# Optimization experiments

Hardware: AMD Instinct MI355X
Metric: run time of the kernel (lower is better)

The kernel has to match this reference:

```python
import jax, jax.numpy as jnp
import numpy as np
import math

D_MODEL = 512
N_HEADS = 8
HEAD_DIM = D_MODEL // N_HEADS


def setup_inputs() -> dict:
    key = jax.random.key(0)
    k1, k2, k3 = jax.random.split(key, 3)
    B, T = 2, 4096
    x = jax.random.normal(k1, (B, T, D_MODEL), dtype=jnp.float32)
    # nn.Linear weights: stored as [out, in], applied as x @ W.T
    W_QKV = jax.random.normal(k2, (3 * D_MODEL, D_MODEL), dtype=jnp.float32) * (1.0 / math.sqrt(D_MODEL))
    W_O = jax.random.normal(k3, (D_MODEL, D_MODEL), dtype=jnp.float32) * (1.0 / math.sqrt(D_MODEL))
    return {"x": x, "W_QKV": W_QKV, "W_O": W_O}


def reference(x, W_QKV, W_O):
    B, T, C = x.shape
    qkv = (x @ W_QKV.T).reshape(B, T, 3, N_HEADS, HEAD_DIM)
    q, k, v = qkv[:, :, 0], qkv[:, :, 1], qkv[:, :, 2]  # [B,T,H,D]
    # scores: [B,H,T,T]
    scale = math.sqrt(HEAD_DIM)
    attn = jnp.einsum('bqhd,bkhd->bhqk', q, k) / scale
    causal_mask = jnp.triu(jnp.ones((T, T), dtype=bool), k=1)
    attn = jnp.where(causal_mask, -jnp.inf, attn)
    attn = jax.nn.softmax(attn, axis=-1)
    out = jnp.einsum('bhqk,bkhd->bqhd', attn, v).reshape(B, T, C)
    return out @ W_O.T
```

## Files before the change

### kernel.cpp

```cpp
#include <hip/hip_runtime.h>
#include <hip/hip_bf16.h>

typedef __bf16 bf16_t;
typedef __bf16 bf16x8 __attribute__((ext_vector_type(8)));
typedef __bf16 bf16x4 __attribute__((ext_vector_type(4)));
typedef float  floatx4 __attribute__((ext_vector_type(4)));

static __device__ __forceinline__ floatx4 mfma16(bf16x8 a, bf16x8 b, floatx4 c) {
  return __builtin_amdgcn_mfma_f32_16x16x32_bf16(a, b, c, 0, 0, 0);
}

typedef __attribute__((address_space(3))) void lds_vp;
typedef __attribute__((address_space(1))) void glb_vp;
#define GLDS16(g, l) \
  __builtin_amdgcn_global_load_lds((glb_vp*)(g), (lds_vp*)(l), 16, 0, 0)

__global__ void cvt_all_kernel(const float* __restrict__ x,
                               const float* __restrict__ wqkv,
                               const float* __restrict__ wo,
                               bf16_t* __restrict__ xb,
                               bf16_t* __restrict__ wqkvb,
                               bf16_t* __restrict__ wob) {
  int i = blockIdx.x * blockDim.x + threadIdx.x;
  const float4* src; bf16x4* dst; int off;
  if (i < 1048576)      { src = (const float4*)x;    dst = (bf16x4*)xb;    off = i; }
  else if (i < 1245184) { src = (const float4*)wqkv; dst = (bf16x4*)wqkvb; off = i - 1048576; }
  else                  { src = (const float4*)wo;   dst = (bf16x4*)wob;   off = i - 1245184; }
  float4 v = src[off];
  bf16x4 o;
  o[0] = (bf16_t)v.x; o[1] = (bf16_t)v.y; o[2] = (bf16_t)v.z; o[3] = (bf16_t)v.w;
  dst[off] = o;
}

__global__ __launch_bounds__(256) void gemm_qkv(
    const bf16_t* __restrict__ A, const bf16_t* __restrict__ B,
    bf16_t* __restrict__ Qo, bf16_t* __restrict__ Ko, bf16_t* __restrict__ Vto)
{
  __shared__ __align__(16) bf16_t As[2][128 * 64];
  __shared__ __align__(16) bf16_t Bs[2][128 * 64];
  const int tid  = threadIdx.x;
  const int lane = tid & 63;
  const int w    = tid >> 6;
  const int quad = lane >> 4;
  const int l15  = lane & 15;
  const int l7   = lane & 7;
  const int wm   = w & 1;
  const int wn   = w >> 1;
  const int K    = 512;

  floatx4 acc[4][4];
  #pragma unroll
  for (int i = 0; i < 4; ++i)
    #pragma unroll
    for (int j = 0; j < 4; ++j)
      acc[i][j] = (floatx4){0.f, 0.f, 0.f, 0.f};

  const bf16_t* Ab = A + (size_t)blockIdx.x * 128 * K;
  const bf16_t* Bb = B + (size_t)blockIdx.y * 128 * K;

  auto stage = [&](int buf, int k0) {
    #pragma unroll
    for (int i = 0; i < 4; ++i) {
      int c = tid + 256 * i;
      int row = c >> 3, colc = c & 7;
      int gofs = ((colc ^ (row & 7)) << 3);
      GLDS16(&Ab[(size_t)row * K + k0 + gofs], &As[buf][c * 8]);
      GLDS16(&Bb[(size_t)row * K + k0 + gofs], &Bs[buf][c * 8]);
    }
  };

  stage(0, 0);
  for (int it = 0; it < 8; ++it) {
    const int cur = it & 1;
    __syncthreads();
    if (it + 1 < 8) stage(cur ^ 1, (it + 1) << 6);
    #pragma unroll
    for (int ks = 0; ks < 2; ++ks) {
      bf16x8 af[4], bfr[4];
      #pragma unroll
      for (int t = 0; t < 4; ++t) {
        af[t]  = *(const bf16x8*)&As[cur][(wm * 64 + t * 16 + l15) * 64 +
                                         (((ks * 4 + quad) ^ l7) << 3)];
        bfr[t] = *(const bf16x8*)&Bs[cur][(wn * 64 + t * 16 + l15) * 64 +
                                         (((ks * 4 + quad) ^ l7) << 3)];
      }
      #pragma unroll
      for (int mt = 0; mt < 4; ++mt)
        #pragma unroll
        for (int nt = 0; nt < 4; ++nt)
          acc[mt][nt] = mfma16(af[mt], bfr[nt], acc[mt][nt]);
    }
  }

  if (blockIdx.y < 8) {
    #pragma unroll
    for (int mt = 0; mt < 4; ++mt) {
      #pragma unroll
      for (int nt = 0; nt < 4; ++nt) {
        #pragma unroll
        for (int r = 0; r < 4; ++r) {
          int m = blockIdx.x * 128 + wm * 64 + mt * 16 + quad * 4 + r;
          int n = blockIdx.y * 128 + wn * 64 + nt * 16 + l15;
          float v = acc[mt][nt][r];
          int b = m >> 12, t = m & 4095;
          int h = (n >> 6) & 7, d = n & 63;
          size_t bh = (size_t)(b * 8 + h);
          if (n < 512)
            Qo[bh * 262144 + (size_t)t * 64 + d] = (bf16_t)(v * 0.18033688f);
          else
            Ko[bh * 262144 +
               (size_t)((((t >> 4) * 2 + (d >> 5)) * 512) +
                        ((((d & 31) >> 3) * 16 + (t & 15)) * 8) + (d & 7))] =
                (bf16_t)v;
        }
      }
    }
  } else {
    __syncthreads();
    bf16_t* L = &As[0][0];
    #pragma unroll
    for (int mt = 0; mt < 4; ++mt)
      #pragma unroll
      for (int nt = 0; nt < 4; ++nt) {
        int n_l = wn * 64 + nt * 16 + l15;
        int mc  = wm * 8 + mt * 2 + (quad >> 1);
        bf16x4 v4;
        #pragma unroll
        for (int r = 0; r < 4; ++r) v4[r] = (bf16_t)acc[mt][nt][r];
        *(bf16x4*)&L[n_l * 128 + ((mc ^ (n_l & 15)) << 3) + (quad & 1) * 4] = v4;
      }
    __syncthreads();
    const int t0 = (blockIdx.x & 31) * 128;
    const int b  = blockIdx.x >> 5;
    #pragma unroll
    for (int i = 0; i < 8; ++i) {
      int c = tid + 256 * i;
      int n_l = c >> 4, tc = c & 15;
      int h = ((blockIdx.y - 8) << 1) | (n_l >> 6);
      int d = n_l & 63;
      size_t bh = (size_t)(b * 8 + h);
      int base0 = (tc >> 2) * 32 + (tc & 3) * 4;
      bf16x4 lo = *(const bf16x4*)&L[n_l * 128 +
                     (((base0 >> 3) ^ (n_l & 15)) << 3) + (base0 & 7)];
      bf16x4 hi = *(const bf16x4*)&L[n_l * 128 +
                     ((((base0 + 16) >> 3) ^ (n_l & 15)) << 3) + (base0 & 7)];
      bf16x8 o;
      #pragma unroll
      for (int e = 0; e < 4; ++e) { o[e] = lo[e]; o[e + 4] = hi[e]; }
      int T = t0 + tc * 8;
      *(bf16x8*)&Vto[bh * 262144 +
                     (size_t)((((T >> 5) * 4 + (d >> 4)) * 512) +
                              ((((T >> 3) & 3) * 16 + (d & 15)) * 8))] = o;
    }
  }
}

__global__ __launch_bounds__(256) void gemm_out(
    const bf16_t* __restrict__ A, const bf16_t* __restrict__ B,
    float* __restrict__ Cf)
{
  __shared__ __align__(16) bf16_t As[2][64 * 64];
  __shared__ __align__(16) bf16_t Bs[2][128 * 64];
  const int tid  = threadIdx.x;
  const int lane = tid & 63;
  const int w    = tid >> 6;
  const int quad = lane >> 4;
  const int l15  = lane & 15;
  const int l7   = lane & 7;

  floatx4 acc[4][2];
  #pragma unroll
  for (int i = 0; i < 4; ++i)
    #pragma unroll
    for (int j = 0; j < 2; ++j)
      acc[i][j] = (floatx4){0.f, 0.f, 0.f, 0.f};

  const bf16_t* Ab = A + (size_t)blockIdx.x * 64 * 512;
  const bf16_t* Bb = B + (size_t)blockIdx.y * 128 * 512;

  auto stage = [&](int buf, int k0) {
    #pragma unroll
    for (int i = 0; i < 2; ++i) {
      int c = tid + 256 * i;
      int row = c >> 3, colc = c & 7;
      GLDS16(&Ab[(size_t)row * 512 + k0 + ((colc ^ (row & 7)) << 3)],
             &As[buf][c * 8]);
    }
    #pragma unroll
    for (int i = 0; i < 4; ++i) {
      int c = tid + 256 * i;
      int row = c >> 3, colc = c & 7;
      GLDS16(&Bb[(size_t)row * 512 + k0 + ((colc ^ (row & 7)) << 3)],
             &Bs[buf][c * 8]);
    }
  };

  stage(0, 0);
  for (int it = 0; it < 8; ++it) {
    const int cur = it & 1;
    __syncthreads();
    if (it + 1 < 8) stage(cur ^ 1, (it + 1) << 6);
    #pragma unroll
    for (int ks = 0; ks < 2; ++ks) {
      bf16x8 af[4], bfr[2];
      #pragma unroll
      for (int t = 0; t < 4; ++t)
        af[t]  = *(const bf16x8*)&As[cur][(t * 16 + l15) * 64 +
                                         (((ks * 4 + quad) ^ l7) << 3)];
      #pragma unroll
      for (int t = 0; t < 2; ++t)
        bfr[t] = *(const bf16x8*)&Bs[cur][(w * 32 + t * 16 + l15) * 64 +
                                         (((ks * 4 + quad) ^ l7) << 3)];
      #pragma unroll
      for (int mt = 0; mt < 4; ++mt)
        #pragma unroll
        for (int nt = 0; nt < 2; ++nt)
          acc[mt][nt] = mfma16(af[mt], bfr[nt], acc[mt][nt]);
    }
  }

  #pragma unroll
  for (int mt = 0; mt < 4; ++mt)
    #pragma unroll
    for (int nt = 0; nt < 2; ++nt)
      #pragma unroll
      for (int r = 0; r < 4; ++r) {
        int m = blockIdx.x * 64 + mt * 16 + quad * 4 + r;
        int n = blockIdx.y * 128 + w * 32 + nt * 16 + l15;
        Cf[(size_t)m * 512 + n] = acc[mt][nt][r];
      }
}

__global__ __launch_bounds__(512, 1) void attn_kernel(
    const bf16_t* __restrict__ Qg, const bf16_t* __restrict__ Kf,
    const bf16_t* __restrict__ Vf, bf16_t* __restrict__ Og)
{
  __shared__ __align__(16) bf16_t smem[66560];

  const int tid  = threadIdx.x;
  const int lane = tid & 63;
  const int w    = tid >> 6;
  const int qh   = w >> 2;
  const int kq   = w & 3;
  const int quad = lane >> 4;
  const int l15  = lane & 15;

  const int id = blockIdx.x;
  const int bh = 2 * (id & 7) + ((id >> 3) & 1);
  const int x  = id >> 4;
  const int qtA = 31 - x, qtB = x;
  const size_t bh_off = (size_t)bh * 262144;
  const int b = bh >> 3, h = bh & 7;

  const bf16_t* Kb_ = Kf + bh_off;
  const bf16_t* Vb_ = Vf + bh_off;
  const floatx4 z4 = (floatx4){0.f, 0.f, 0.f, 0.f};
  bf16x8 ones;
  #pragma unroll
  for (int i = 0; i < 8; ++i) ones[i] = (bf16_t)1.0f;

  for (int ph = 0; ph < 2; ++ph) {
    const int qt   = ph ? qtB : qtA;
    const int q64  = 2 * qt + qh;
    const int qbase = qt * 128 + qh * 64;

    bf16x8 aq0[4], aq1[4];
    #pragma unroll
    for (int qb = 0; qb < 4; ++qb) {
      const bf16_t* Qp = Qg + bh_off + (size_t)(qbase + qb * 16 + l15) * 64;
      aq0[qb] = *(const bf16x8*)&Qp[quad * 8];
      aq1[qb] = *(const bf16x8*)&Qp[32 + quad * 8];
    }

    floatx4 acc_o[4][4], acc_l[4];
    #pragma unroll
    for (int qb = 0; qb < 4; ++qb) {
      #pragma unroll
      for (int dt = 0; dt < 4; ++dt) acc_o[qb][dt] = (floatx4){0.f, 0.f, 0.f, 0.f};
      acc_l[qb] = (floatx4){0.f, 0.f, 0.f, 0.f};
    }

    for (int k64 = kq; k64 <= q64; k64 += 4) {
      const bf16_t* Kp = Kb_ + (size_t)k64 * 4096;
      const bf16_t* Vp = Vb_ + (size_t)k64 * 4096;
      bf16x8 bk0[4], bk1[4];
      #pragma unroll
      for (int nt = 0; nt < 4; ++nt) {
        bk0[nt] = *(const bf16x8*)&Kp[(nt * 2 + 0) * 512 + lane * 8];
        bk1[nt] = *(const bf16x8*)&Kp[(nt * 2 + 1) * 512 + lane * 8];
      }
      floatx4 s[4][4];
      #pragma unroll
      for (int nt = 0; nt < 4; ++nt) {
        s[0][nt] = mfma16(bk0[nt], aq0[0], z4);
        s[1][nt] = mfma16(bk0[nt], aq0[1], z4);
        s[2][nt] = mfma16(bk0[nt], aq0[2], z4);
        s[3][nt] = mfma16(bk0[nt], aq0[3], z4);
      }
      #pragma unroll
      for (int nt = 0; nt < 4; ++nt)
        #pragma unroll
        for (int qb = 0; qb < 4; ++qb)
          s[qb][nt] = mfma16(bk1[nt], aq1[qb], s[qb][nt]);
      bf16x8 av[2][4];
      #pragma unroll
      for (int kc = 0; kc < 2; ++kc)
        #pragma unroll
        for (int dt = 0; dt < 4; ++dt)
          av[kc][dt] = *(const bf16x8*)&Vp[(kc * 4 + dt) * 512 + lane * 8];
      if (k64 == q64) {
        #pragma unroll
        for (int qb = 0; qb < 4; ++qb)
          #pragma unroll
          for (int nt = 0; nt < 4; ++nt)
            #pragma unroll
            for (int r = 0; r < 4; ++r)
              if (nt * 16 + quad * 4 + r > qb * 16 + l15)
                s[qb][nt][r] = -3.0e38f;
      }
      #pragma unroll
      for (int qb = 0; qb < 4; ++qb)
        #pragma unroll
        for (int nt = 0; nt < 4; ++nt)
          #pragma unroll
          for (int r = 0; r < 4; ++r)
            s[qb][nt][r] = __builtin_amdgcn_exp2f(s[qb][nt][r]);
      #pragma unroll
      for (int kc = 0; kc < 2; ++kc) {
        bf16x8 pb[4];
        #pragma unroll
        for (int qb = 0; qb < 4; ++qb)
          #pragma unroll
          for (int r = 0; r < 4; ++r) {
            pb[qb][r]     = (bf16_t)s[qb][kc * 2][r];
            pb[qb][r + 4] = (bf16_t)s[qb][kc * 2 + 1][r];
          }
        #pragma unroll
        for (int qb = 0; qb < 4; ++qb)
          acc_l[qb] = mfma16(ones, pb[qb], acc_l[qb]);
        #pragma unroll
        for (int dt = 0; dt < 4; ++dt)
          #pragma unroll
          for (int qb = 0; qb < 4; ++qb)
            acc_o[qb][dt] = mfma16(av[kc][dt], pb[qb], acc_o[qb][dt]);
      }
    }

    {
      float* Pq = (float*)&smem[0] + (qh * 4 + kq) * 4096;
      float* PL = (float*)&smem[65536];
      #pragma unroll
      for (int qb = 0; qb < 4; ++qb) {
        int q = qb * 16 + l15;
        #pragma unroll
        for (int dt = 0; dt < 4; ++dt)
          *(floatx4*)&Pq[q * 64 + (((dt * 4 + quad) ^ l15) << 2)] = acc_o[qb][dt];
        if (quad == 0) PL[(qh * 4 + kq) * 64 + q] = acc_l[qb][0];
      }
    }
    __syncthreads();
    #pragma unroll
    for (int i = 0; i < 2; ++i) {
      int a = tid + 512 * i;
      int qh_e = a >> 9, rem = a & 511;
      int q = rem >> 3, c8 = rem & 7;
      const float* Pq = (const float*)&smem[0] + qh_e * 16384;
      const float* PL = (const float*)&smem[65536] + qh_e * 256;
      float s0[8] = {0.f, 0.f, 0.f, 0.f, 0.f, 0.f, 0.f, 0.f};
      float suml = 0.f;
      #pragma unroll
      for (int k2 = 0; k2 < 4; ++k2) {
        const float* Pk = Pq + k2 * 4096 + q * 64;
        floatx4 u0 = *(const floatx4*)&Pk[((c8 * 2)     ^ (q & 15)) << 2];
        floatx4 u1 = *(const floatx4*)&Pk[((c8 * 2 + 1) ^ (q & 15)) << 2];
        #pragma unroll
        for (int r = 0; r < 4; ++r) { s0[r] += u0[r]; s0[4 + r] += u1[r]; }
        suml += PL[k2 * 64 + q];
      }
      float rl = 1.0f / suml;
      bf16x8 o;
      #pragma unroll
      for (int e = 0; e < 8; ++e) o[e] = (bf16_t)(s0[e] * rl);
      int row = qt * 128 + qh_e * 64 + q;
      *(bf16x8*)&Og[((size_t)b * 4096 + row) * 512 + h * 64 + c8 * 8] = o;
    }
    if (ph == 0) __syncthreads();
  }
}

extern "C" void kernel_launch(void* const* d_in, const int* in_sizes, int n_in,
                              void* d_out, int out_size, void* d_ws, size_t ws_size,
                              hipStream_t stream) {
  const float* x    = (const float*)d_in[0];
  const float* wqkv = (const float*)d_in[1];
  const float* wo   = (const float*)d_in[2];
  float* out = (float*)d_out;

  char* ws = (char*)d_ws;
  bf16_t* xb    = (bf16_t*)(ws);
  bf16_t* wqkvb = (bf16_t*)(ws + 8388608);
  bf16_t* wob   = (bf16_t*)(ws + 9961472);
  bf16_t* Qb    = (bf16_t*)(ws + 10485760);
  bf16_t* Kfb   = (bf16_t*)(ws + 18874368);
  bf16_t* Vfb   = (bf16_t*)(ws + 27262976);
  bf16_t* Ob    = xb;

  cvt_all_kernel<<<5120, 256, 0, stream>>>(x, wqkv, wo, xb, wqkvb, wob);

  gemm_qkv<<<dim3(64, 12), 256, 0, stream>>>(xb, wqkvb, Qb, Kfb, Vfb);
  attn_kernel<<<dim3(256), 512, 0, stream>>>(Qb, Kfb, Vfb, Ob);
  gemm_out<<<dim3(128, 4), 256, 0, stream>>>(Ob, wob, out);
}
```

Before: 144.8 us.

## Split attention work across 8 KV-slices per 64-row query tile with 512 blocks

Each attention block now owns a single 64-row query tile per phase instead of a 128-row pair, and all eight waves split the key range (stride 8) rather than two query halves with four key slices each. The grid doubles to 512 blocks, and the launch bound is raised to allow multiple blocks per CU. Shared memory is roughly halved by reducing the partial outputs in two head-dimension halves with extra barriers. The aim is better load balance and occupancy across the GPU, at the cost of more cross-wave reductions and synchronization, and Q/K reuse across waves within a block.

Result: slower. 457.2 us (+215.8%).

```diff
diff --git a/kernel.cpp b/kernel.cpp
--- a/kernel.cpp
+++ b/kernel.cpp
@@ -231,24 +231,22 @@
       }
 }
 
-__global__ __launch_bounds__(512, 1) void attn_kernel(
+__global__ __launch_bounds__(512, 4) void attn_kernel(
     const bf16_t* __restrict__ Qg, const bf16_t* __restrict__ Kf,
     const bf16_t* __restrict__ Vf, bf16_t* __restrict__ Og)
 {
-  __shared__ __align__(16) bf16_t smem[66560];
+  __shared__ __align__(16) bf16_t smem[33792];
 
   const int tid  = threadIdx.x;
   const int lane = tid & 63;
-  const int w    = tid >> 6;
-  const int qh   = w >> 2;
-  const int kq   = w & 3;
+  const int kq   = tid >> 6;
   const int quad = lane >> 4;
   const int l15  = lane & 15;
 
   const int id = blockIdx.x;
   const int bh = 2 * (id & 7) + ((id >> 3) & 1);
-  const int x  = id >> 4;
-  const int qtA = 31 - x, qtB = x;
+  const int y  = id >> 4;
+  const int q64A = 63 - y, q64B = y;
   const size_t bh_off = (size_t)bh * 262144;
   const int b = bh >> 3, h = bh & 7;
 
@@ -260,9 +258,8 @@
   for (int i = 0; i < 8; ++i) ones[i] = (bf16_t)1.0f;
 
   for (int ph = 0; ph < 2; ++ph) {
-    const int qt   = ph ? qtB : qtA;
-    const int q64  = 2 * qt + qh;
-    const int qbase = qt * 128 + qh * 64;
+    const int q64 = ph ? q64B : q64A;
+    const int qbase = q64 * 64;
 
     bf16x8 aq0[4], aq1[4];
     #pragma unroll
@@ -280,7 +277,7 @@
       acc_l[qb] = (floatx4){0.f, 0.f, 0.f, 0.f};
     }
 
-    for (int k64 = kq; k64 <= q64; k64 += 4) {
+    for (int k64 = kq; k64 <= q64; k64 += 8) {
       const bf16_t* Kp = Kb_ + (size_t)k64 * 4096;
       const bf16_t* Vp = Vb_ + (size_t)k64 * 4096;
       bf16x8 bk0[4], bk1[4];
@@ -346,45 +343,46 @@
       }
     }
 
-    {
-      float* Pq = (float*)&smem[0] + (qh * 4 + kq) * 4096;
-      float* PL = (float*)&smem[65536];
-      #pragma unroll
-      for (int qb = 0; qb < 4; ++qb) {
-        int q = qb * 16 + l15;
-        #pragma unroll
-        for (int dt = 0; dt < 4; ++dt)
-          *(floatx4*)&Pq[q * 64 + (((dt * 4 + quad) ^ l15) << 2)] = acc_o[qb][dt];
-        if (quad == 0) PL[(qh * 4 + kq) * 64 + q] = acc_l[qb][0];
-      }
-    }
-    __syncthreads();
-    #pragma unroll
-    for (int i = 0; i < 2; ++i) {
-      int a = tid + 512 * i;
-      int qh_e = a >> 9, rem = a & 511;
-      int q = rem >> 3, c8 = rem & 7;
-      const float* Pq = (const float*)&smem[0] + qh_e * 16384;
-      const float* PL = (const float*)&smem[65536] + qh_e * 256;
-      float s0[8] = {0.f, 0.f, 0.f, 0.f, 0.f, 0.f, 0.f, 0.f};
-      float suml = 0.f;
-      #pragma unroll
-      for (int k2 = 0; k2 < 4; ++k2) {
-        const float* Pk = Pq + k2 * 4096 + q * 64;
-        floatx4 u0 = *(const floatx4*)&Pk[((c8 * 2)     ^ (q & 15)) << 2];
-        floatx4 u1 = *(const floatx4*)&Pk[((c8 * 2 + 1) ^ (q & 15)) << 2];
-        #pragma unroll
-        for (int r = 0; r < 4; ++r) { s0[r] += u0[r]; s0[4 + r] += u1[r]; }
-        suml += PL[k2 * 64 + q];
-      }
-      float rl = 1.0f / suml;
-      bf16x8 o;
-      #pragma unroll
-      for (int e = 0; e < 8; ++e) o[e] = (bf16_t)(s0[e] * rl);
-      int row = qt * 128 + qh_e * 64 + q;
-      *(bf16x8*)&Og[((size_t)b * 4096 + row) * 512 + h * 64 + c8 * 8] = o;
-    }
-    if (ph == 0) __syncthreads();
+    #pragma unroll
+    for (int hd = 0; hd < 2; ++hd) {
+      if (ph | hd) __syncthreads();
+      {
+        float* Pw  = (float*)&smem[0] + kq * 2048;
+        float* PLw = (float*)&smem[32768];
+        #pragma unroll
+        for (int qb = 0; qb < 4; ++qb) {
+          int q = qb * 16 + l15;
+          #pragma unroll
+          for (int t = 0; t < 2; ++t) {
+            int cw = (t * 4 + quad) ^ (q & 7);
+            *(floatx4*)&Pw[q * 32 + cw * 4] = acc_o[qb][hd * 2 + t];
+          }
+          if (hd == 0 && quad == 0) PLw[kq * 64 + q] = acc_l[qb][0];
+        }
+      }
+      __syncthreads();
+      {
+        int q = tid >> 3, c = tid & 7;
+        const float* PB = (const float*)&smem[0];
+        const float* PL = (const float*)&smem[32768];
+        floatx4 ssum = (floatx4){0.f, 0.f, 0.f, 0.f};
+        float suml = 0.f;
+        #pragma unroll
+        for (int k = 0; k < 8; ++k) {
+          const float* Pk = PB + k * 2048 + q * 32;
+          floatx4 u = *(const floatx4*)&Pk[(c ^ (q & 7)) * 4];
+          #pragma unroll
+          for (int r = 0; r < 4; ++r) ssum[r] += u[r];
+          suml += PL[k * 64 + q];
+        }
+        float rl = 1.0f / suml;
+        bf16x4 o4;
+        #pragma unroll
+        for (int r = 0; r < 4; ++r) o4[r] = (bf16_t)(ssum[r] * rl);
+        int row = qbase + q;
+        *(bf16x4*)&Og[((size_t)b * 4096 + row) * 512 + h * 64 + hd * 32 + c * 4] = o4;
+      }
+    }
   }
 }
 
@@ -408,6 +406,6 @@
   cvt_all_kernel<<<5120, 256, 0, stream>>>(x, wqkv, wo, xb, wqkvb, wob);
 
   gemm_qkv<<<dim3(64, 12), 256, 0, stream>>>(xb, wqkvb, Qb, Kfb, Vfb);
-  attn_kernel<<<dim3(256), 512, 0, stream>>>(Qb, Kfb, Vfb, Ob);
+  attn_kernel<<<dim3(512), 512, 0, stream>>>(Qb, Kfb, Vfb, Ob);
   gemm_out<<<dim3(128, 4), 256, 0, stream>>>(Ob, wob, out);
 }
```

## Fuse fp32-to-bf16 conversion of x into the QKV GEMM A-tile load

Applied to the files above, without the earlier changes.

The x activation is no longer converted to bf16 by a separate pass. The QKV GEMM now loads fp32 x tiles into registers, converts them, and writes them into swizzled LDS after the MFMA loop, as a register-staged software pipeline. Only the weights still go through a smaller conversion kernel. This removes an 8 MB write and read of bf16 x, but each of the 12 column blocks now reads x as fp32 (twice the bytes), and the kernel uses more registers and VALU work.

Result: slower. 152.7 us (+5.5%).

```diff
diff --git a/kernel.cpp b/kernel.cpp
--- a/kernel.cpp
+++ b/kernel.cpp
@@ -15,17 +15,14 @@
 #define GLDS16(g, l) \
   __builtin_amdgcn_global_load_lds((glb_vp*)(g), (lds_vp*)(l), 16, 0, 0)
 
-__global__ void cvt_all_kernel(const float* __restrict__ x,
-                               const float* __restrict__ wqkv,
-                               const float* __restrict__ wo,
-                               bf16_t* __restrict__ xb,
-                               bf16_t* __restrict__ wqkvb,
-                               bf16_t* __restrict__ wob) {
+__global__ void cvt_w_kernel(const float* __restrict__ wqkv,
+                             const float* __restrict__ wo,
+                             bf16_t* __restrict__ wqkvb,
+                             bf16_t* __restrict__ wob) {
   int i = blockIdx.x * blockDim.x + threadIdx.x;
   const float4* src; bf16x4* dst; int off;
-  if (i < 1048576)      { src = (const float4*)x;    dst = (bf16x4*)xb;    off = i; }
-  else if (i < 1245184) { src = (const float4*)wqkv; dst = (bf16x4*)wqkvb; off = i - 1048576; }
-  else                  { src = (const float4*)wo;   dst = (bf16x4*)wob;   off = i - 1245184; }
+  if (i < 196608) { src = (const float4*)wqkv; dst = (bf16x4*)wqkvb; off = i; }
+  else            { src = (const float4*)wo;   dst = (bf16x4*)wob;   off = i - 196608; }
   float4 v = src[off];
   bf16x4 o;
   o[0] = (bf16_t)v.x; o[1] = (bf16_t)v.y; o[2] = (bf16_t)v.z; o[3] = (bf16_t)v.w;
@@ -33,7 +30,7 @@
 }
 
 __global__ __launch_bounds__(256) void gemm_qkv(
-    const bf16_t* __restrict__ A, const bf16_t* __restrict__ B,
+    const float* __restrict__ A, const bf16_t* __restrict__ B,
     bf16_t* __restrict__ Qo, bf16_t* __restrict__ Ko, bf16_t* __restrict__ Vto)
 {
   __shared__ __align__(16) bf16_t As[2][128 * 64];
@@ -55,25 +52,51 @@
     for (int j = 0; j < 4; ++j)
       acc[i][j] = (floatx4){0.f, 0.f, 0.f, 0.f};
 
-  const bf16_t* Ab = A + (size_t)blockIdx.x * 128 * K;
+  const float*  Ab = A + (size_t)blockIdx.x * 128 * K;
   const bf16_t* Bb = B + (size_t)blockIdx.y * 128 * K;
 
-  auto stage = [&](int buf, int k0) {
+  float4 ar[4][2];
+  auto loadA = [&](int k0) {
     #pragma unroll
     for (int i = 0; i < 4; ++i) {
       int c = tid + 256 * i;
       int row = c >> 3, colc = c & 7;
-      int gofs = ((colc ^ (row & 7)) << 3);
-      GLDS16(&Ab[(size_t)row * K + k0 + gofs], &As[buf][c * 8]);
-      GLDS16(&Bb[(size_t)row * K + k0 + gofs], &Bs[buf][c * 8]);
+      const float* pa = &Ab[(size_t)row * K + k0 + ((colc ^ (row & 7)) << 3)];
+      ar[i][0] = *(const float4*)pa;
+      ar[i][1] = *(const float4*)(pa + 4);
     }
   };
-
-  stage(0, 0);
+  auto writeA = [&](int buf) {
+    #pragma unroll
+    for (int i = 0; i < 4; ++i) {
+      int c = tid + 256 * i;
+      bf16x8 av;
+      av[0] = (bf16_t)ar[i][0].x; av[1] = (bf16_t)ar[i][0].y;
+      av[2] = (bf16_t)ar[i][0].z; av[3] = (bf16_t)ar[i][0].w;
+      av[4] = (bf16_t)ar[i][1].x; av[5] = (bf16_t)ar[i][1].y;
+      av[6] = (bf16_t)ar[i][1].z; av[7] = (bf16_t)ar[i][1].w;
+      *(bf16x8*)&As[buf][c * 8] = av;
+    }
+  };
+  auto stageB = [&](int buf, int k0) {
+    #pragma unroll
+    for (int i = 0; i < 4; ++i) {
+      int c = tid + 256 * i;
+      int row = c >> 3, colc = c & 7;
+      GLDS16(&Bb[(size_t)row * K + k0 + ((colc ^ (row & 7)) << 3)], &Bs[buf][c * 8]);
+    }
+  };
+
+  loadA(0);
+  writeA(0);
+  stageB(0, 0);
   for (int it = 0; it < 8; ++it) {
     const int cur = it & 1;
     __syncthreads();
-    if (it + 1 < 8) stage(cur ^ 1, (it + 1) << 6);
+    if (it + 1 < 8) {
+      stageB(cur ^ 1, (it + 1) << 6);
+      loadA((it + 1) << 6);
+    }
     #pragma unroll
     for (int ks = 0; ks < 2; ++ks) {
       bf16x8 af[4], bfr[4];
@@ -90,6 +113,7 @@
         for (int nt = 0; nt < 4; ++nt)
           acc[mt][nt] = mfma16(af[mt], bfr[nt], acc[mt][nt]);
     }
+    if (it + 1 < 8) writeA(cur ^ 1);
   }
 
   if (blockIdx.y < 8) {
@@ -397,17 +421,16 @@
   float* out = (float*)d_out;
 
   char* ws = (char*)d_ws;
-  bf16_t* xb    = (bf16_t*)(ws);
+  bf16_t* Ob    = (bf16_t*)(ws);
   bf16_t* wqkvb = (bf16_t*)(ws + 8388608);
   bf16_t* wob   = (bf16_t*)(ws + 9961472);
   bf16_t* Qb    = (bf16_t*)(ws + 10485760);
   bf16_t* Kfb   = (bf16_t*)(ws + 18874368);
   bf16_t* Vfb   = (bf16_t*)(ws + 27262976);
-  bf16_t* Ob    = xb;
-
-  cvt_all_kernel<<<5120, 256, 0, stream>>>(x, wqkv, wo, xb, wqkvb, wob);
-
-  gemm_qkv<<<dim3(64, 12), 256, 0, stream>>>(xb, wqkvb, Qb, Kfb, Vfb);
+
+  cvt_w_kernel<<<1024, 256, 0, stream>>>(wqkv, wo, wqkvb, wob);
+
+  gemm_qkv<<<dim3(64, 12), 256, 0, stream>>>(x, wqkvb, Qb, Kfb, Vfb);
   attn_kernel<<<dim3(256), 512, 0, stream>>>(Qb, Kfb, Vfb, Ob);
   gemm_out<<<dim3(128, 4), 256, 0, stream>>>(Ob, wob, out);
 }
```
